# Kernel optimization log

Measured on AMD Instinct MI355X. Metric: run time of the kernel, lower is better.

Reference implementation:

```python
import jax, jax.numpy as jnp
import numpy as np
from math import sqrt

P = 1.0  # axis-aligned transform exponent (init arg p)
EPS = 1e-6


def setup_inputs() -> dict:
    key = jax.random.key(0)
    k1, k2, k3, k4 = jax.random.split(key, 4)
    B, L, S, H, E = 4, 2048, 2048, 8, 64
    return {
        "queries": jax.random.normal(k1, (B, L, H, E), dtype=jnp.float32),
        "keys": jax.random.normal(k2, (B, S, H, E), dtype=jnp.float32),
        "values": jax.random.normal(k3, (B, S, H, E), dtype=jnp.float32),
        "attn_mask": jnp.zeros((1, 1, 1, 1), dtype=bool),  # unused: mask_flag=False
        "directional_weights": jnp.ones((1, 1, 1, 1), dtype=jnp.float32),
        "dynamic_param": jax.random.normal(k4, (1,), dtype=jnp.float32),
    }


def _transform(x, directional_weights, dynamic_param):
    # axis_aligned_transformation: rescale by (1/std over seq dim)^p (unbiased std, like torch)
    std = jnp.std(x, axis=-2, keepdims=True, ddof=1)
    x = x * (1.0 / (std + EPS)) ** P
    # directional_reweighting then nonlinear_mapping
    x = x * directional_weights
    return jnp.tanh(x) * dynamic_param


def reference(queries, keys, values, attn_mask, directional_weights, dynamic_param):
    B, L, H, E = queries.shape
    scale = 1.0 / sqrt(E)
    qt = _transform(queries, directional_weights, dynamic_param)  # [B,L,H,E]
    kt = _transform(keys, directional_weights, dynamic_param)     # [B,S,H,E]
    scores = jnp.einsum('blhe,bshe->bhls', qt, kt)                # [B,H,L,S]
    # per-row tau = sqrt(var(scores) + eps), unbiased variance like torch.var
    tau = jnp.sqrt(jnp.var(scores, axis=-1, keepdims=True, ddof=1) + EPS)
    A = jax.nn.softmax(scale * scores / tau, axis=-1)             # [B,H,L,S]
    V = jnp.einsum('bhls,bshd->blhd', A, values)                  # [B,L,H,D]
    return V
```

## Files before the change

### kernel.cpp

```cpp
#include <hip/hip_runtime.h>
#include <math.h>

#define B_ 4
#define L_ 2048
#define S_ 2048
#define H_ 8
#define E_ 64
#define BH_ (B_*H_)
#define EPS 1e-6f

typedef __attribute__((ext_vector_type(8))) short short8;
typedef __attribute__((ext_vector_type(4))) float f32x4;

__device__ __forceinline__ unsigned short f2bf(float f) {
    unsigned int u = __float_as_uint(f);
    u = (u + 0x7fffu + ((u >> 16) & 1u)) >> 16;
    return (unsigned short)u;
}

__device__ __forceinline__ float bf2f(unsigned short u) {
    return __uint_as_float(((unsigned int)u) << 16);
}

__device__ __forceinline__ float fast_tanh(float x) {
    float e = __expf(2.0f * x);
    return 1.0f - 2.0f / (e + 1.0f);
}

__device__ __forceinline__ int swb(int row, int byteoff) {
    return row * 128 + ((((byteoff >> 4) ^ (row & 7)) << 4) | (byteoff & 15));
}

__global__ __launch_bounds__(256) void pre_kernel(
    const float* __restrict__ xq, const float* __restrict__ xk,
    const float* __restrict__ xv,
    unsigned short* __restrict__ qt, unsigned short* __restrict__ kt,
    unsigned short* __restrict__ vt,
    const float* __restrict__ dwp, const float* __restrict__ dpp)
{
    __shared__ float ls[64][65];
    int bx = blockIdx.x;
    if (bx < 4096) {
        const float* x = (bx < 2048) ? xq : xk;
        unsigned short* xt = (bx < 2048) ? qt : kt;
        int g = (bx & 2047) * 256 + threadIdx.x;
        int e = g & 63;
        int bl = g >> 6;
        int b = bl >> 11;
        int l = bl & 2047;
        size_t base = (size_t)bl * (H_ * E_) + e;
        float v[8], s = 0.f, q = 0.f;
#pragma unroll
        for (int h = 0; h < 8; ++h) {
            float t = x[base + h * E_];
            v[h] = t; s += t; q += t * t;
        }
        float mean = s * 0.125f;
        float var = (q - s * mean) * (1.f / 7.f);
        var = fmaxf(var, 0.f);
        float inv = 1.f / (sqrtf(var) + EPS);
        float wsc = dwp[0] * inv;
        float d = dpp[0];
#pragma unroll
        for (int h = 0; h < 8; ++h) {
            float t = fast_tanh(v[h] * wsc) * d;
            xt[((size_t)(b * H_ + h) * L_ + l) * E_ + e] = f2bf(t);
        }
    } else {
        int t2 = bx - 4096;
        int s0 = (t2 & 31) * 64;
        int h = (t2 >> 5) & 7, b = t2 >> 8;
        int t = threadIdx.x;
#pragma unroll
        for (int i = 0; i < 4; ++i) {
            int idx = t + i * 256;
            int r = idx >> 4, c4 = (idx & 15) * 4;
            const float4 f = *(const float4*)&xv[((size_t)(b * S_ + s0 + r) * H_ + h) * E_ + c4];
            ls[r][c4] = f.x; ls[r][c4 + 1] = f.y; ls[r][c4 + 2] = f.z; ls[r][c4 + 3] = f.w;
        }
        __syncthreads();
        size_t ob = ((size_t)(b * H_ + h) * (S_ / 64) + (s0 >> 6)) * 4096;
#pragma unroll
        for (int i = 0; i < 2; ++i) {
            int ri = t + i * 256;
            int et = ri >> 7, c = (ri >> 6) & 1, quad = (ri >> 4) & 3, m = ri & 15;
            int e = et * 16 + m, sb = c * 32 + quad * 8;
            unsigned short tmp[8];
#pragma unroll
            for (int j = 0; j < 8; ++j) tmp[j] = f2bf(ls[sb + j][e]);
            *(uint4*)&vt[ob + (size_t)ri * 8] = *(uint4*)tmp;
        }
    }
}

__global__ __launch_bounds__(256) void gram_kernel(
    const unsigned short* __restrict__ kt, unsigned short* __restrict__ Gb,
    float* __restrict__ ksum)
{
    __shared__ unsigned short ks[128 * 72];
    __shared__ float gs[4096];
    __shared__ float kss[64];
    int bh = blockIdx.x;
    const unsigned short* base = kt + (size_t)bh * S_ * E_;
    int tid = threadIdx.x, lane = tid & 63, w = tid >> 6;
    int m = lane & 15, quad = lane >> 4;

    f32x4 acc[4][4];
#pragma unroll
    for (int i = 0; i < 4; ++i)
#pragma unroll
        for (int j = 0; j < 4; ++j) acc[i][j] = (f32x4){0.f, 0.f, 0.f, 0.f};
    float ksp[4] = {0.f, 0.f, 0.f, 0.f};

    short8 stg[4];
#pragma unroll
    for (int i = 0; i < 4; ++i)
        stg[i] = *(const short8*)(base + (size_t)(tid + i * 256) * 8);

    for (int ch = 0; ch < 16; ++ch) {
        __syncthreads();
#pragma unroll
        for (int i = 0; i < 4; ++i) {
            int u = tid + i * 256;
            *(short8*)&ks[(u >> 3) * 72 + (u & 7) * 8] = stg[i];
        }
        __syncthreads();
        if (ch < 15) {
#pragma unroll
            for (int i = 0; i < 4; ++i)
                stg[i] = *(const short8*)(base + (size_t)(ch + 1) * 8192 + (tid + i * 256) * 8);
        }
        int s0 = w * 32;
        short8 af[4];
#pragma unroll
        for (int i = 0; i < 4; ++i) {
            short8 a;
#pragma unroll
            for (int kk = 0; kk < 8; ++kk) {
                unsigned short uv = ks[(s0 + quad * 8 + kk) * 72 + i * 16 + m];
                a[kk] = (short)uv;
                ksp[i] += bf2f(uv);
            }
            af[i] = a;
        }
#pragma unroll
        for (int i = 0; i < 4; ++i)
#pragma unroll
            for (int j = 0; j < 4; ++j)
                acc[i][j] = __builtin_amdgcn_mfma_f32_16x16x32_bf16(af[i], af[j], acc[i][j], 0, 0, 0);
    }
#pragma unroll
    for (int i = 0; i < 4; ++i) {
        ksp[i] += __shfl_xor(ksp[i], 16);
        ksp[i] += __shfl_xor(ksp[i], 32);
    }
    for (int w2 = 0; w2 < 4; ++w2) {
        if (w == w2) {
#pragma unroll
            for (int i = 0; i < 4; ++i)
#pragma unroll
                for (int j = 0; j < 4; ++j)
#pragma unroll
                    for (int r = 0; r < 4; ++r) {
                        int idx = (i * 16 + quad * 4 + r) * 64 + j * 16 + m;
                        if (w2 == 0) gs[idx] = acc[i][j][r]; else gs[idx] += acc[i][j][r];
                    }
            if (lane < 16) {
#pragma unroll
                for (int i = 0; i < 4; ++i) {
                    int e = i * 16 + lane;
                    if (w2 == 0) kss[e] = ksp[i]; else kss[e] += ksp[i];
                }
            }
        }
        __syncthreads();
    }
#pragma unroll
    for (int ii = 0; ii < 16; ++ii) {
        int idx = tid + ii * 256;
        Gb[(size_t)bh * 4096 + idx] = f2bf(gs[idx]);
    }
    if (tid < 64) ksum[bh * 64 + tid] = kss[tid];
}

__global__ __launch_bounds__(256, 2) void attn_kernel(
    const unsigned short* __restrict__ qt,
    const unsigned short* __restrict__ kt,
    const unsigned short* __restrict__ vt,
    const unsigned short* __restrict__ Gb,
    const float* __restrict__ ksum,
    float* __restrict__ out)
{
    __shared__ __align__(16) char lds[33792];
    const int tid = threadIdx.x;
    const int lane = tid & 63;
    const int w = tid >> 6;
    const int m = lane & 15;
    const int quad = lane >> 4;
    char* ptb = lds + 16384 + w * 4096;
    float2* ascr = (float2*)(lds + 32768) + w * 32;

    int blk = blockIdx.x;
    int bh = (blk & 7) * 4 + ((blk >> 3) & 3);
    int l0 = (blk >> 5) * 128;
    int b = bh >> 3, h = bh & 7;

    const unsigned short* qtb = qt + (size_t)bh * L_ * E_;
    const unsigned short* ktb = kt + (size_t)bh * S_ * E_;
    const unsigned short* vtb = vt + (size_t)bh * (S_ / 64) * 4096;

    short8 qf[2][2];
#pragma unroll
    for (int g = 0; g < 2; ++g)
#pragma unroll
        for (int c = 0; c < 2; ++c)
            qf[g][c] = *(const short8*)(qtb + (size_t)(l0 + w * 32 + g * 16 + m) * E_ + c * 32 + quad * 8);

    float al[2], alm[2];
    {
        const unsigned short* gb = Gb + (size_t)bh * 4096;
        short8 gfr[4][2];
#pragma unroll
        for (int j = 0; j < 4; ++j)
#pragma unroll
            for (int c = 0; c < 2; ++c)
                gfr[j][c] = *(const short8*)(gb + (size_t)(j * 16 + m) * 64 + c * 32 + quad * 8);
        float ksl[4];
#pragma unroll
        for (int j = 0; j < 4; ++j) ksl[j] = ksum[bh * 64 + j * 16 + m];
#pragma unroll
        for (int g = 0; g < 2; ++g) {
            f32x4 accj[4];
#pragma unroll
            for (int j = 0; j < 4; ++j) {
                accj[j] = (f32x4){0.f, 0.f, 0.f, 0.f};
#pragma unroll
                for (int c = 0; c < 2; ++c)
                    accj[j] = __builtin_amdgcn_mfma_f32_16x16x32_bf16(qf[g][c], gfr[j][c], accj[j], 0, 0, 0);
            }
            float ps[4] = {0, 0, 0, 0}, pr[4] = {0, 0, 0, 0};
#pragma unroll
            for (int r = 0; r < 4; ++r)
#pragma unroll
                for (int j = 0; j < 4; ++j) {
                    float qv = bf2f(qtb[(size_t)(l0 + w * 32 + g * 16 + quad * 4 + r) * E_ + j * 16 + m]);
                    ps[r] = fmaf(accj[j][r], qv, ps[r]);
                    pr[r] = fmaf(qv, ksl[j], pr[r]);
                }
#pragma unroll
            for (int mask = 1; mask < 16; mask <<= 1)
#pragma unroll
                for (int r = 0; r < 4; ++r) {
                    ps[r] += __shfl_xor(ps[r], mask);
                    pr[r] += __shfl_xor(pr[r], mask);
                }
            if (m == 0) {
#pragma unroll
                for (int r = 0; r < 4; ++r) {
                    float sum = pr[r];
                    float mu = sum * (1.f / S_);
                    float var = (ps[r] - sum * mu) * (1.f / (S_ - 1));
                    var = fmaxf(var, 0.f);
                    float tau = sqrtf(var + EPS);
                    float a = 0.125f / tau;
                    ascr[g * 16 + quad * 4 + r] = make_float2(a, a * mu);
                }
            }
        }
#pragma unroll
        for (int g = 0; g < 2; ++g) {
            float2 a2 = ascr[g * 16 + m];
            al[g] = a2.x; alm[g] = a2.y;
        }
    }

    float dsum[2] = {0.f, 0.f};
    f32x4 oacc[2][4];
#pragma unroll
    for (int g = 0; g < 2; ++g)
#pragma unroll
        for (int et = 0; et < 4; ++et) oacc[g][et] = (f32x4){0.f, 0.f, 0.f, 0.f};

    uint4 kr[2];
#pragma unroll
    for (int i = 0; i < 2; ++i)
        kr[i] = *(const uint4*)(ktb + (size_t)(tid + i * 256) * 8);
#pragma unroll
    for (int i = 0; i < 2; ++i) {
        int u = tid + i * 256;
        *(uint4*)(lds + swb(u >> 3, (u & 7) * 16)) = kr[i];
    }
    __syncthreads();

    for (int st = 0; st < S_ / 64; ++st) {
        char* kcur = lds + (st & 1) * 8192;
        char* knxt = lds + ((st + 1) & 1) * 8192;
        if (st < S_ / 64 - 1) {
#pragma unroll
            for (int i = 0; i < 2; ++i)
                kr[i] = *(const uint4*)(ktb + (size_t)(st + 1) * 4096 + (size_t)(tid + i * 256) * 8);
        }
        const unsigned short* vstb = vtb + (size_t)st * 4096;
        short8 vf[2][4];
#pragma unroll
        for (int c = 0; c < 2; ++c)
#pragma unroll
            for (int et = 0; et < 4; ++et)
                vf[c][et] = *(const short8*)(vstb + et * 1024 + c * 512 + lane * 8);

#pragma unroll
        for (int nt = 0; nt < 4; ++nt) {
            short8 kf0 = *(const short8*)(kcur + swb(nt * 16 + m, quad * 16));
            short8 kf1 = *(const short8*)(kcur + swb(nt * 16 + m, 64 + quad * 16));
#pragma unroll
            for (int g = 0; g < 2; ++g) {
                f32x4 acc = {0.f, 0.f, 0.f, 0.f};
                acc = __builtin_amdgcn_mfma_f32_16x16x32_bf16(kf0, qf[g][0], acc, 0, 0, 0);
                acc = __builtin_amdgcn_mfma_f32_16x16x32_bf16(kf1, qf[g][1], acc, 0, 0, 0);
                unsigned int u0, u1, u2, u3;
                {
                    float p0 = __expf(fmaf(al[g], acc[0], -alm[g]));
                    float p1 = __expf(fmaf(al[g], acc[1], -alm[g]));
                    float p2 = __expf(fmaf(al[g], acc[2], -alm[g]));
                    float p3 = __expf(fmaf(al[g], acc[3], -alm[g]));
                    u0 = __float_as_uint(p0) & 0xffff0000u;
                    u1 = __float_as_uint(p1) & 0xffff0000u;
                    u2 = __float_as_uint(p2) & 0xffff0000u;
                    u3 = __float_as_uint(p3) & 0xffff0000u;
                    dsum[g] += __uint_as_float(u0) + __uint_as_float(u1)
                             + __uint_as_float(u2) + __uint_as_float(u3);
                }
                uint2 pk;
                pk.x = (u0 >> 16) | u1;
                pk.y = (u2 >> 16) | u3;
                *(uint2*)(ptb + swb(g * 16 + m, nt * 32 + quad * 8)) = pk;
            }
        }
#pragma unroll
        for (int g = 0; g < 2; ++g) {
            short8 pf0 = *(const short8*)(ptb + swb(g * 16 + m, quad * 16));
            short8 pf1 = *(const short8*)(ptb + swb(g * 16 + m, 64 + quad * 16));
#pragma unroll
            for (int et = 0; et < 4; ++et) {
                oacc[g][et] = __builtin_amdgcn_mfma_f32_16x16x32_bf16(pf0, vf[0][et], oacc[g][et], 0, 0, 0);
                oacc[g][et] = __builtin_amdgcn_mfma_f32_16x16x32_bf16(pf1, vf[1][et], oacc[g][et], 0, 0, 0);
            }
        }
        if (st < S_ / 64 - 1) {
#pragma unroll
            for (int i = 0; i < 2; ++i) {
                int u = tid + i * 256;
                *(uint4*)(knxt + swb(u >> 3, (u & 7) * 16)) = kr[i];
            }
        }
        __syncthreads();
    }

#pragma unroll
    for (int g = 0; g < 2; ++g) {
        dsum[g] += __shfl_xor(dsum[g], 16);
        dsum[g] += __shfl_xor(dsum[g], 32);
    }
#pragma unroll
    for (int g = 0; g < 2; ++g) {
#pragma unroll
        for (int r = 0; r < 4; ++r) {
            float dn = __shfl(dsum[g], quad * 4 + r);
            float rd = 1.0f / dn;
            size_t row = (size_t)(b * L_ + l0 + w * 32 + g * 16 + quad * 4 + r);
#pragma unroll
            for (int et = 0; et < 4; ++et)
                out[(row * H_ + h) * E_ + et * 16 + m] = oacc[g][et][r] * rd;
        }
    }
}

extern "C" void kernel_launch(void* const* d_in, const int* in_sizes, int n_in,
                              void* d_out, int out_size, void* d_ws, size_t ws_size,
                              hipStream_t stream)
{
    const float* q = (const float*)d_in[0];
    const float* k = (const float*)d_in[1];
    const float* v = (const float*)d_in[2];
    const float* dw = (const float*)d_in[4];
    const float* dp = (const float*)d_in[5];
    float* out = (float*)d_out;

    unsigned short* qt = (unsigned short*)d_ws;
    unsigned short* kt = qt + (size_t)BH_ * L_ * E_;
    unsigned short* vt = kt + (size_t)BH_ * S_ * E_;
    unsigned short* Gb = vt + (size_t)BH_ * E_ * S_;
    float* ksum = (float*)(Gb + (size_t)BH_ * 4096);

    pre_kernel<<<5120, 256, 0, stream>>>(q, k, v, qt, kt, vt, dw, dp);
    gram_kernel<<<BH_, 256, 0, stream>>>(kt, Gb, ksum);
    attn_kernel<<<512, 256, 0, stream>>>(qt, kt, vt, Gb, ksum, out);
}
```

Measured before the change: 175.8 us.

## Split attention block into 8 waves of 16 rows each

The attention kernel now runs 512 threads per block: 8 waves each handle 16 query rows instead of 4 waves handling 32, and each thread stages a single K vector per tile. Per-wave state (Q fragments, accumulators, denominators) is halved, and LDS offsets are precomputed, with the loop unrolled by two to remove the buffer-select arithmetic. The aim is to raise latency hiding and occupancy, at the cost that each K tile and each V fragment is now loaded by twice as many waves per row group, so reuse per load drops.

```diff
diff --git a/kernel.cpp b/kernel.cpp
--- a/kernel.cpp
+++ b/kernel.cpp
@@ -183,7 +183,7 @@
     if (tid < 64) ksum[bh * 64 + tid] = kss[tid];
 }
 
-__global__ __launch_bounds__(256, 2) void attn_kernel(
+__global__ __launch_bounds__(512, 4) void attn_kernel(
     const unsigned short* __restrict__ qt,
     const unsigned short* __restrict__ kt,
     const unsigned short* __restrict__ vt,
@@ -197,8 +197,8 @@
     const int w = tid >> 6;
     const int m = lane & 15;
     const int quad = lane >> 4;
-    char* ptb = lds + 16384 + w * 4096;
-    float2* ascr = (float2*)(lds + 32768) + w * 32;
+    char* ptb = lds + 16384 + w * 2048;
+    float2* ascr = (float2*)(lds + 32768) + w * 16;
 
     int blk = blockIdx.x;
     int bh = (blk & 7) * 4 + ((blk >> 3) & 3);
@@ -209,14 +209,12 @@
     const unsigned short* ktb = kt + (size_t)bh * S_ * E_;
     const unsigned short* vtb = vt + (size_t)bh * (S_ / 64) * 4096;
 
-    short8 qf[2][2];
-#pragma unroll
-    for (int g = 0; g < 2; ++g)
-#pragma unroll
-        for (int c = 0; c < 2; ++c)
-            qf[g][c] = *(const short8*)(qtb + (size_t)(l0 + w * 32 + g * 16 + m) * E_ + c * 32 + quad * 8);
-
-    float al[2], alm[2];
+    short8 qf[2];
+#pragma unroll
+    for (int c = 0; c < 2; ++c)
+        qf[c] = *(const short8*)(qtb + (size_t)(l0 + w * 16 + m) * E_ + c * 32 + quad * 8);
+
+    float al, alm;
     {
         const unsigned short* gb = Gb + (size_t)bh * 4096;
         short8 gfr[4][2];
@@ -228,78 +226,66 @@
         float ksl[4];
 #pragma unroll
         for (int j = 0; j < 4; ++j) ksl[j] = ksum[bh * 64 + j * 16 + m];
-#pragma unroll
-        for (int g = 0; g < 2; ++g) {
-            f32x4 accj[4];
+        f32x4 accj[4];
+#pragma unroll
+        for (int j = 0; j < 4; ++j) {
+            accj[j] = (f32x4){0.f, 0.f, 0.f, 0.f};
+            accj[j] = __builtin_amdgcn_mfma_f32_16x16x32_bf16(qf[0], gfr[j][0], accj[j], 0, 0, 0);
+            accj[j] = __builtin_amdgcn_mfma_f32_16x16x32_bf16(qf[1], gfr[j][1], accj[j], 0, 0, 0);
+        }
+        float ps[4] = {0, 0, 0, 0}, pr[4] = {0, 0, 0, 0};
+#pragma unroll
+        for (int r = 0; r < 4; ++r)
 #pragma unroll
             for (int j = 0; j < 4; ++j) {
-                accj[j] = (f32x4){0.f, 0.f, 0.f, 0.f};
-#pragma unroll
-                for (int c = 0; c < 2; ++c)
-                    accj[j] = __builtin_amdgcn_mfma_f32_16x16x32_bf16(qf[g][c], gfr[j][c], accj[j], 0, 0, 0);
-            }
-            float ps[4] = {0, 0, 0, 0}, pr[4] = {0, 0, 0, 0};
-#pragma unroll
-            for (int r = 0; r < 4; ++r)
-#pragma unroll
-                for (int j = 0; j < 4; ++j) {
-                    float qv = bf2f(qtb[(size_t)(l0 + w * 32 + g * 16 + quad * 4 + r) * E_ + j * 16 + m]);
-                    ps[r] = fmaf(accj[j][r], qv, ps[r]);
-                    pr[r] = fmaf(qv, ksl[j], pr[r]);
-                }
-#pragma unroll
-            for (int mask = 1; mask < 16; mask <<= 1)
-#pragma unroll
-                for (int r = 0; r < 4; ++r) {
-                    ps[r] += __shfl_xor(ps[r], mask);
-                    pr[r] += __shfl_xor(pr[r], mask);
-                }
-            if (m == 0) {
-#pragma unroll
-                for (int r = 0; r < 4; ++r) {
-                    float sum = pr[r];
-                    float mu = sum * (1.f / S_);
-                    float var = (ps[r] - sum * mu) * (1.f / (S_ - 1));
-                    var = fmaxf(var, 0.f);
-                    float tau = sqrtf(var + EPS);
-                    float a = 0.125f / tau;
-                    ascr[g * 16 + quad * 4 + r] = make_float2(a, a * mu);
-                }
-            }
-        }
-#pragma unroll
-        for (int g = 0; g < 2; ++g) {
-            float2 a2 = ascr[g * 16 + m];
-            al[g] = a2.x; alm[g] = a2.y;
-        }
-    }
-
-    float dsum[2] = {0.f, 0.f};
-    f32x4 oacc[2][4];
-#pragma unroll
-    for (int g = 0; g < 2; ++g)
-#pragma unroll
-        for (int et = 0; et < 4; ++et) oacc[g][et] = (f32x4){0.f, 0.f, 0.f, 0.f};
-
-    uint4 kr[2];
-#pragma unroll
-    for (int i = 0; i < 2; ++i)
-        kr[i] = *(const uint4*)(ktb + (size_t)(tid + i * 256) * 8);
-#pragma unroll
-    for (int i = 0; i < 2; ++i) {
-        int u = tid + i * 256;
-        *(uint4*)(lds + swb(u >> 3, (u & 7) * 16)) = kr[i];
-    }
+                float qv = bf2f(qtb[(size_t)(l0 + w * 16 + quad * 4 + r) * E_ + j * 16 + m]);
+                ps[r] = fmaf(accj[j][r], qv, ps[r]);
+                pr[r] = fmaf(qv, ksl[j], pr[r]);
+            }
+#pragma unroll
+        for (int mask = 1; mask < 16; mask <<= 1)
+#pragma unroll
+            for (int r = 0; r < 4; ++r) {
+                ps[r] += __shfl_xor(ps[r], mask);
+                pr[r] += __shfl_xor(pr[r], mask);
+            }
+        if (m == 0) {
+#pragma unroll
+            for (int r = 0; r < 4; ++r) {
+                float sum = pr[r];
+                float mu = sum * (1.f / S_);
+                float var = (ps[r] - sum * mu) * (1.f / (S_ - 1));
+                var = fmaxf(var, 0.f);
+                float tau = sqrtf(var + EPS);
+                float a = 0.125f / tau;
+                ascr[quad * 4 + r] = make_float2(a, a * mu);
+            }
+        }
+        float2 a2 = ascr[m];
+        al = a2.x; alm = a2.y;
+    }
+
+    float dsum = 0.f;
+    f32x4 oacc[4];
+#pragma unroll
+    for (int et = 0; et < 4; ++et) oacc[et] = (f32x4){0.f, 0.f, 0.f, 0.f};
+
+    int ko[4], pw[4];
+#pragma unroll
+    for (int nt = 0; nt < 4; ++nt) {
+        ko[nt] = swb(nt * 16 + m, quad * 16);
+        pw[nt] = swb(m, nt * 32 + quad * 8);
+    }
+    const int pr0 = swb(m, quad * 16);
+    const int stg = swb(tid >> 3, (tid & 7) * 16);
+
+    uint4 kr = *(const uint4*)(ktb + (size_t)tid * 8);
+    *(uint4*)(lds + stg) = kr;
     __syncthreads();
 
-    for (int st = 0; st < S_ / 64; ++st) {
-        char* kcur = lds + (st & 1) * 8192;
-        char* knxt = lds + ((st + 1) & 1) * 8192;
-        if (st < S_ / 64 - 1) {
-#pragma unroll
-            for (int i = 0; i < 2; ++i)
-                kr[i] = *(const uint4*)(ktb + (size_t)(st + 1) * 4096 + (size_t)(tid + i * 256) * 8);
-        }
+    auto step = [&](int st, char* kcur, char* knxt) {
+        if (st < S_ / 64 - 1)
+            kr = *(const uint4*)(ktb + (size_t)(st + 1) * 4096 + (size_t)tid * 8);
         const unsigned short* vstb = vtb + (size_t)st * 4096;
         short8 vf[2][4];
 #pragma unroll
@@ -310,68 +296,56 @@
 
 #pragma unroll
         for (int nt = 0; nt < 4; ++nt) {
-            short8 kf0 = *(const short8*)(kcur + swb(nt * 16 + m, quad * 16));
-            short8 kf1 = *(const short8*)(kcur + swb(nt * 16 + m, 64 + quad * 16));
-#pragma unroll
-            for (int g = 0; g < 2; ++g) {
-                f32x4 acc = {0.f, 0.f, 0.f, 0.f};
-                acc = __builtin_amdgcn_mfma_f32_16x16x32_bf16(kf0, qf[g][0], acc, 0, 0, 0);
-                acc = __builtin_amdgcn_mfma_f32_16x16x32_bf16(kf1, qf[g][1], acc, 0, 0, 0);
-                unsigned int u0, u1, u2, u3;
-                {
-                    float p0 = __expf(fmaf(al[g], acc[0], -alm[g]));
-                    float p1 = __expf(fmaf(al[g], acc[1], -alm[g]));
-                    float p2 = __expf(fmaf(al[g], acc[2], -alm[g]));
-                    float p3 = __expf(fmaf(al[g], acc[3], -alm[g]));
-                    u0 = __float_as_uint(p0) & 0xffff0000u;
-                    u1 = __float_as_uint(p1) & 0xffff0000u;
-                    u2 = __float_as_uint(p2) & 0xffff0000u;
-                    u3 = __float_as_uint(p3) & 0xffff0000u;
-                    dsum[g] += __uint_as_float(u0) + __uint_as_float(u1)
-                             + __uint_as_float(u2) + __uint_as_float(u3);
-                }
-                uint2 pk;
-                pk.x = (u0 >> 16) | u1;
-                pk.y = (u2 >> 16) | u3;
-                *(uint2*)(ptb + swb(g * 16 + m, nt * 32 + quad * 8)) = pk;
-            }
-        }
-#pragma unroll
-        for (int g = 0; g < 2; ++g) {
-            short8 pf0 = *(const short8*)(ptb + swb(g * 16 + m, quad * 16));
-            short8 pf1 = *(const short8*)(ptb + swb(g * 16 + m, 64 + quad * 16));
-#pragma unroll
-            for (int et = 0; et < 4; ++et) {
-                oacc[g][et] = __builtin_amdgcn_mfma_f32_16x16x32_bf16(pf0, vf[0][et], oacc[g][et], 0, 0, 0);
-                oacc[g][et] = __builtin_amdgcn_mfma_f32_16x16x32_bf16(pf1, vf[1][et], oacc[g][et], 0, 0, 0);
-            }
-        }
-        if (st < S_ / 64 - 1) {
-#pragma unroll
-            for (int i = 0; i < 2; ++i) {
-                int u = tid + i * 256;
-                *(uint4*)(knxt + swb(u >> 3, (u & 7) * 16)) = kr[i];
-            }
-        }
-        __syncthreads();
-    }
-
-#pragma unroll
-    for (int g = 0; g < 2; ++g) {
-        dsum[g] += __shfl_xor(dsum[g], 16);
-        dsum[g] += __shfl_xor(dsum[g], 32);
-    }
-#pragma unroll
-    for (int g = 0; g < 2; ++g) {
-#pragma unroll
-        for (int r = 0; r < 4; ++r) {
-            float dn = __shfl(dsum[g], quad * 4 + r);
-            float rd = 1.0f / dn;
-            size_t row = (size_t)(b * L_ + l0 + w * 32 + g * 16 + quad * 4 + r);
-#pragma unroll
-            for (int et = 0; et < 4; ++et)
-                out[(row * H_ + h) * E_ + et * 16 + m] = oacc[g][et][r] * rd;
-        }
+            short8 kf0 = *(const short8*)(kcur + ko[nt]);
+            short8 kf1 = *(const short8*)(kcur + (ko[nt] ^ 64));
+            f32x4 acc = (f32x4){0.f, 0.f, 0.f, 0.f};
+            acc = __builtin_amdgcn_mfma_f32_16x16x32_bf16(kf0, qf[0], acc, 0, 0, 0);
+            acc = __builtin_amdgcn_mfma_f32_16x16x32_bf16(kf1, qf[1], acc, 0, 0, 0);
+            unsigned int u0, u1, u2, u3;
+            {
+                float p0 = __expf(fmaf(al, acc[0], -alm));
+                float p1 = __expf(fmaf(al, acc[1], -alm));
+                float p2 = __expf(fmaf(al, acc[2], -alm));
+                float p3 = __expf(fmaf(al, acc[3], -alm));
+                u0 = __float_as_uint(p0) & 0xffff0000u;
+                u1 = __float_as_uint(p1) & 0xffff0000u;
+                u2 = __float_as_uint(p2) & 0xffff0000u;
+                u3 = __float_as_uint(p3) & 0xffff0000u;
+                dsum += __uint_as_float(u0) + __uint_as_float(u1)
+                      + __uint_as_float(u2) + __uint_as_float(u3);
+            }
+            uint2 pk;
+            pk.x = (u0 >> 16) | u1;
+            pk.y = (u2 >> 16) | u3;
+            *(uint2*)(ptb + pw[nt]) = pk;
+        }
+        short8 pf0 = *(const short8*)(ptb + pr0);
+        short8 pf1 = *(const short8*)(ptb + (pr0 ^ 64));
+#pragma unroll
+        for (int et = 0; et < 4; ++et) {
+            oacc[et] = __builtin_amdgcn_mfma_f32_16x16x32_bf16(pf0, vf[0][et], oacc[et], 0, 0, 0);
+            oacc[et] = __builtin_amdgcn_mfma_f32_16x16x32_bf16(pf1, vf[1][et], oacc[et], 0, 0, 0);
+        }
+        if (st < S_ / 64 - 1)
+            *(uint4*)(knxt + stg) = kr;
+        __syncthreads();
+    };
+#pragma unroll 1
+    for (int st2 = 0; st2 < S_ / 128; ++st2) {
+        step(2 * st2,     lds,        lds + 8192);
+        step(2 * st2 + 1, lds + 8192, lds);
+    }
+
+    dsum += __shfl_xor(dsum, 16);
+    dsum += __shfl_xor(dsum, 32);
+#pragma unroll
+    for (int r = 0; r < 4; ++r) {
+        float dn = __shfl(dsum, quad * 4 + r);
+        float rd = 1.0f / dn;
+        size_t row = (size_t)(b * L_ + l0 + w * 16 + quad * 4 + r);
+#pragma unroll
+        for (int et = 0; et < 4; ++et)
+            out[(row * H_ + h) * E_ + et * 16 + m] = oacc[et][r] * rd;
     }
 }
 
@@ -394,5 +368,5 @@
 
     pre_kernel<<<5120, 256, 0, stream>>>(q, k, v, qt, kt, vt, dw, dp);
     gram_kernel<<<BH_, 256, 0, stream>>>(kt, Gb, ksum);
-    attn_kernel<<<512, 256, 0, stream>>>(qt, kt, vt, Gb, ksum, out);
-}
+    attn_kernel<<<512, 512, 0, stream>>>(qt, kt, vt, Gb, ksum, out);
+}
```

Result: faster. 171.6 us (-2.4%).
